# Optimization experiments

Hardware: AMD Instinct MI355X
Metric: run time of the kernel (lower is better)

## Reference

```python
import jax, jax.numpy as jnp
import numpy as np
from jax import lax

B, C, H, W = 4, 256, 64, 64
C8 = C // 8


def _conv1x1(x, w, b):
    # x: (B,C,H,W), w: (O,C) -> (B,O,H,W)
    return jnp.einsum('bchw,oc->bohw', x, w) + b[None, :, None, None]


def setup_inputs() -> dict:
    key = jax.random.key(0)
    ks = jax.random.split(key, 9)
    s1 = 1.0 / np.sqrt(C)          # fan-in scale for 1x1 convs
    sf = 1.0 / np.sqrt(2 * C * 9)  # fan-in scale for 3x3 conv
    return {
        'front_x':     jax.random.normal(ks[0], (B, C, H, W), jnp.float32),
        'cross_x':     jax.random.normal(ks[1], (B, C, H, W), jnp.float32),
        'front_x_hat': jax.random.normal(ks[2], (B, C, H, W), jnp.float32),
        'Wq': jax.random.normal(ks[3], (C8, C), jnp.float32) * s1,
        'bq': jnp.zeros((C8,), jnp.float32),
        'Wk': jax.random.normal(ks[4], (C8, C), jnp.float32) * s1,
        'bk': jnp.zeros((C8,), jnp.float32),
        'Wv': jax.random.normal(ks[5], (C, C), jnp.float32) * s1,
        'bv': jnp.zeros((C,), jnp.float32),
        'Wf': jax.random.normal(ks[6], (C, 2 * C, 3, 3), jnp.float32) * sf,
        'bf': jnp.zeros((C,), jnp.float32),
    }


def reference(front_x, cross_x, front_x_hat, Wq, bq, Wk, bk, Wv, bv, Wf, bf):
    b, c, h, w = front_x.shape
    hw = h * w
    # projections -> (B, C/8, HW)
    q = _conv1x1(cross_x, Wq, bq).reshape(b, -1, hw)
    k = _conv1x1(front_x, Wk, bk).reshape(b, -1, hw)
    # energy[b,i,j] = <key_i, query_j>  (B, HW, HW)
    energy = jnp.einsum('bci,bcj->bij', k, q)
    front_star = jnp.max(energy, axis=1)     # (B, HW) best key score per query
    front_arg = jnp.argmax(energy, axis=1)   # (B, HW) best key index per query
    # value projection and hard gather of best-matching value per position
    v = _conv1x1(front_x_hat, Wv, bv).reshape(b, c, hw)
    T = jnp.take_along_axis(v, front_arg[:, None, :], axis=2).reshape(b, c, h, w)
    S = front_star.reshape(b, 1, h, w)
    cat = jnp.concatenate([front_x, T], axis=1)  # (B, 2C, H, W)
    res = lax.conv_general_dilated(
        cat, Wf, window_strides=(1, 1), padding='SAME',
        dimension_numbers=('NCHW', 'OIHW', 'NCHW')) + bf[None, :, None, None]
    return front_x + res * S
```

## Files before the change

kernel.cpp:

```cpp
#include <hip/hip_runtime.h>

#define Bn 4
#define Cn 256
#define C8 32
#define Hn 64
#define Wn 64
#define HWn 4096
#define PADR 80
#define ROWS (HWn + 2 * PADR)
#define MARGIN 6e-3f

typedef __bf16 bf16x8 __attribute__((ext_vector_type(8)));
typedef float floatx4 __attribute__((ext_vector_type(4)));
typedef unsigned short u16x8 __attribute__((ext_vector_type(8)));

__device__ __forceinline__ unsigned short f2bf(float f) {
  union { float f; unsigned int u; } c; c.f = f;
  unsigned int u = c.u;
  return (unsigned short)((u + 0x7FFFu + ((u >> 16) & 1u)) >> 16);
}
__device__ __forceinline__ float bf2f(unsigned short h) {
  union { unsigned int u; float f; } c; c.u = ((unsigned int)h) << 16;
  return c.f;
}
__device__ __forceinline__ void gl_lds16(const void* g, void* l) {
  __builtin_amdgcn_global_load_lds(
      (__attribute__((address_space(1))) void*)(uintptr_t)g,
      (__attribute__((address_space(3))) void*)(uintptr_t)l, 16, 0, 0);
}

__global__ void prep_w(const float* __restrict__ Wq, const float* __restrict__ Wk,
                       const float* __restrict__ Wv, const float* __restrict__ Wf,
                       float* __restrict__ Wqf, float* __restrict__ Wkf,
                       unsigned short* __restrict__ Wvb, unsigned short* __restrict__ Wfb,
                       int* __restrict__ cnt) {
  size_t t = (size_t)blockIdx.x * 256 + threadIdx.x;
  if (t == 0) cnt[0] = 0;
  if (t < 8192) {
    int o = (int)(t / 256), c = (int)(t % 256);
    Wqf[(size_t)c * 32 + o] = Wq[t];
    Wkf[(size_t)c * 32 + o] = Wk[t];
  }
  if (t < 65536) Wvb[t] = f2bf(Wv[t]);
  if (t < (size_t)9 * 256 * 512) {
    int tap = (int)(t / (256 * 512));
    int rem = (int)(t % (256 * 512));
    int o = rem / 512, ci = rem % 512;
    Wfb[t] = f2bf(Wf[((size_t)o * 512 + ci) * 9 + tap]);
  }
}

__global__ __launch_bounds__(1024) void proj_qk(
    const float* __restrict__ cross_x, const float* __restrict__ front_x,
    const float* __restrict__ Wqf, const float* __restrict__ bq,
    const float* __restrict__ Wkf, const float* __restrict__ bk,
    float* __restrict__ qf, float* __restrict__ kf,
    unsigned short* __restrict__ qhi, unsigned short* __restrict__ qlo,
    unsigned short* __restrict__ khi, unsigned short* __restrict__ klo) {
  int tid = threadIdx.x;
  int lane = tid & 63, wv = tid >> 6;
  int slice = wv & 3;
  int chunk = wv >> 2;
  int j = blockIdx.x * 64 + lane;
  int b = blockIdx.y;
  int z = blockIdx.z;
  const float* x = (z == 0) ? cross_x : front_x;
  const float* Wg = (z == 0) ? Wqf : Wkf;
  const float* bd = (z == 0) ? bq : bk;
  float* outp = (z == 0) ? qf : kf;
  unsigned short* hip_ = (z == 0) ? qhi : khi;
  unsigned short* lop_ = (z == 0) ? qlo : klo;
  int o0 = slice * 8;
  int c0 = chunk * 64;

  __shared__ __align__(16) float Wl[8192];
  __shared__ float part[3 * 4 * 8 * 64];

  for (int u = tid; u < 8192; u += 1024) Wl[u] = Wg[u];
  __syncthreads();

  const float* xb = x + (size_t)b * Cn * HWn + j;
  floatx4 a0 = (floatx4)0.0f, a1 = (floatx4)0.0f;
#pragma unroll 16
  for (int c = c0; c < c0 + 64; ++c) {
    float xv = xb[(size_t)c * HWn];
    floatx4 wa = *reinterpret_cast<const floatx4*>(&Wl[c * 32 + o0]);
    floatx4 wb = *reinterpret_cast<const floatx4*>(&Wl[c * 32 + o0 + 4]);
    a0 += wa * xv;
    a1 += wb * xv;
  }
  if (chunk > 0) {
    float* dst = &part[(((chunk - 1) * 4 + slice) * 8) * 64];
#pragma unroll
    for (int o = 0; o < 4; ++o) { dst[o * 64 + lane] = a0[o]; dst[(o + 4) * 64 + lane] = a1[o]; }
  }
  __syncthreads();
  if (chunk != 0) return;
#pragma unroll
  for (int q = 0; q < 3; ++q) {
    const float* src = &part[((q * 4 + slice) * 8) * 64];
#pragma unroll
    for (int o = 0; o < 4; ++o) { a0[o] += src[o * 64 + lane]; a1[o] += src[(o + 4) * 64 + lane]; }
  }
  float acc[8];
#pragma unroll
  for (int o = 0; o < 4; ++o) { acc[o] = a0[o] + bd[o0 + o]; acc[o + 4] = a1[o] + bd[o0 + 4 + o]; }

  float* op = outp + ((size_t)b * HWn + j) * C8 + o0;
  u16x8 hv, lv;
#pragma unroll
  for (int o = 0; o < 8; ++o) {
    op[o] = acc[o];
    unsigned short h = f2bf(acc[o]);
    hv[o] = h;
    lv[o] = f2bf(acc[o] - bf2f(h));
  }
  *reinterpret_cast<u16x8*>(hip_ + ((size_t)b * HWn + j) * C8 + o0) = hv;
  *reinterpret_cast<u16x8*>(lop_ + ((size_t)b * HWn + j) * C8 + o0) = lv;
}

__global__ __launch_bounds__(1024) void energy_approx(
    const unsigned short* __restrict__ khi, const unsigned short* __restrict__ klo,
    const unsigned short* __restrict__ qhi, const unsigned short* __restrict__ qlo,
    float* __restrict__ star, int* __restrict__ argb,
    int* __restrict__ cnt, int* __restrict__ list) {
  int b = blockIdx.y;
  int j0 = blockIdx.x * 32;
  int tid = threadIdx.x;
  int lane = tid & 63, wv = tid >> 6;
  int lm = lane & 15, lq = lane >> 4;

  __shared__ float bv1S[16][32];
  __shared__ int   bi1S[16][32];
  __shared__ float bv2S[16][32];

  bf16x8 qh[2], ql[2];
#pragma unroll
  for (int s = 0; s < 2; ++s) {
    int j = j0 + s * 16 + lm;
    qh[s] = *reinterpret_cast<const bf16x8*>(qhi + ((size_t)b * HWn + j) * 32 + lq * 8);
    ql[s] = *reinterpret_cast<const bf16x8*>(qlo + ((size_t)b * HWn + j) * 32 + lq * 8);
  }
  const unsigned short* kh_base = khi + (size_t)b * HWn * 32 + lq * 8;
  const unsigned short* kl_base = klo + (size_t)b * HWn * 32 + lq * 8;

  float b1[2], b2[2];
#pragma unroll
  for (int s = 0; s < 2; ++s) { b1[s] = -3.0e38f; b2[s] = -3.0e38f; }

  int ibase = wv * 256;
#pragma unroll 4
  for (int it = 0; it < 16; ++it) {
    int i0 = ibase + it * 16;
    bf16x8 ah = *reinterpret_cast<const bf16x8*>(kh_base + (size_t)(i0 + lm) * 32);
    bf16x8 al = *reinterpret_cast<const bf16x8*>(kl_base + (size_t)(i0 + lm) * 32);
#pragma unroll
    for (int s = 0; s < 2; ++s) {
      floatx4 acc = (floatx4)0.0f;
      acc = __builtin_amdgcn_mfma_f32_16x16x32_bf16(ah, qh[s], acc, 0, 0, 0);
      acc = __builtin_amdgcn_mfma_f32_16x16x32_bf16(ah, ql[s], acc, 0, 0, 0);
      acc = __builtin_amdgcn_mfma_f32_16x16x32_bf16(al, qh[s], acc, 0, 0, 0);
#pragma unroll
      for (int r = 0; r < 4; ++r) {
        unsigned code = (unsigned)(it * 4 + r);
        union { float f; unsigned u; } cv; cv.f = acc[r];
        cv.u = (cv.u & ~63u) | code;
        float vp = cv.f;
        b2[s] = __builtin_amdgcn_fmed3f(vp, b1[s], b2[s]);
        b1[s] = fmaxf(b1[s], vp);
      }
    }
  }
  int i1[2];
#pragma unroll
  for (int s = 0; s < 2; ++s) {
    union { float f; unsigned u; } cv; cv.f = b1[s];
    unsigned code = cv.u & 63u;
    i1[s] = ibase + (int)(code >> 2) * 16 + lq * 4 + (int)(code & 3u);
  }
#pragma unroll
  for (int s = 0; s < 2; ++s) {
#pragma unroll
    for (int m = 16; m <= 32; m <<= 1) {
      float ob1 = __shfl_xor(b1[s], m, 64);
      int oi1 = __shfl_xor(i1[s], m, 64);
      float ob2 = __shfl_xor(b2[s], m, 64);
      float c2;
      if (ob1 > b1[s] || (ob1 == b1[s] && oi1 < i1[s])) {
        c2 = fmaxf(b1[s], ob2);
        b1[s] = ob1; i1[s] = oi1;
      } else {
        c2 = fmaxf(ob1, b2[s]);
      }
      b2[s] = c2;
    }
    if (lq == 0) {
      bv1S[wv][s * 16 + lm] = b1[s];
      bi1S[wv][s * 16 + lm] = i1[s];
      bv2S[wv][s * 16 + lm] = b2[s];
    }
  }
  __syncthreads();
  if (tid < 32) {
    float B1 = bv1S[0][tid];
    int I1 = bi1S[0][tid];
    float B2 = bv2S[0][tid];
#pragma unroll
    for (int w = 1; w < 16; ++w) {
      float v1 = bv1S[w][tid];
      int ii = bi1S[w][tid];
      float v2 = bv2S[w][tid];
      if (v1 > B1) { B2 = fmaxf(B1, v2); B1 = v1; I1 = ii; }
      else B2 = fmaxf(B2, v1);
    }
    size_t o = (size_t)b * HWn + j0 + tid;
    union { float f; unsigned u; } cs; cs.f = B1;
    cs.u &= ~63u;
    star[o] = cs.f;
    argb[o] = I1;
    if (B1 - B2 < MARGIN) {
      int slot = atomicAdd(cnt, 1);
      list[slot] = (b << 12) | (j0 + (int)tid);
    }
  }
}

__global__ __launch_bounds__(256) void recheck(
    const float* __restrict__ qf, const float* __restrict__ kf,
    const int* __restrict__ cnt, const int* __restrict__ list,
    float* __restrict__ star, int* __restrict__ argb) {
  __shared__ double bvS[4];
  __shared__ int biS[4];
  int n = cnt[0];
  int tid = threadIdx.x;
  int lane = tid & 63, wv = tid >> 6;
  for (int idx = blockIdx.x; idx < n; idx += gridDim.x) {
    int e = list[idx];
    int b = e >> 12, j = e & 4095;
    const float* qp = qf + ((size_t)b * HWn + j) * 32;
    double qj[32];
#pragma unroll
    for (int o = 0; o < 32; ++o) qj[o] = (double)qp[o];
    double best = -1.0e300;
    int bi = 1 << 30;
    for (int i = tid; i < HWn; i += 256) {
      const float* kp = kf + ((size_t)b * HWn + i) * 32;
      double s = 0.0;
#pragma unroll
      for (int o = 0; o < 32; ++o) s += (double)kp[o] * qj[o];
      if (s > best) { best = s; bi = i; }
    }
#pragma unroll
    for (int m = 1; m < 64; m <<= 1) {
      double ob = __shfl_xor(best, m, 64);
      int oi = __shfl_xor(bi, m, 64);
      if (ob > best || (ob == best && oi < bi)) { best = ob; bi = oi; }
    }
    if (lane == 0) { bvS[wv] = best; biS[wv] = bi; }
    __syncthreads();
    if (tid == 0) {
#pragma unroll
      for (int w = 1; w < 4; ++w) {
        if (bvS[w] > best || (bvS[w] == best && biS[w] < bi)) {
          best = bvS[w]; bi = biS[w];
        }
      }
      star[(size_t)b * HWn + j] = (float)best;
      argb[(size_t)b * HWn + j] = bi;
    }
    __syncthreads();
  }
}

__global__ __launch_bounds__(256) void cat_fx(
    const float* __restrict__ fx, const float* __restrict__ fxh,
    unsigned short* __restrict__ catC, unsigned short* __restrict__ xht) {
  int j0 = blockIdx.x * 64;
  int ci0 = blockIdx.y * 64;
  int b = blockIdx.z >> 1;
  int which = blockIdx.z & 1;
  int tid = threadIdx.x;
  __shared__ unsigned short tile[64][66];

  const float* src = (which == 0) ? fx : fxh;
  for (int u = tid; u < 4096; u += 256) {
    int cl = u >> 6, hw_l = u & 63;
    tile[cl][hw_l] = f2bf(src[((size_t)(b * Cn + ci0 + cl)) * HWn + j0 + hw_l]);
  }
  __syncthreads();
  if (which == 0) {
    for (int u = tid; u < 4096; u += 256) {
      int hw_l = u >> 6, cl = u & 63;
      catC[((size_t)b * ROWS + PADR + j0 + hw_l) * 512 + ci0 + cl] = tile[cl][hw_l];
    }
  } else {
    for (int u = tid; u < 4096; u += 256) {
      int hw_l = u >> 6, cl = u & 63;
      xht[((size_t)b * HWn + j0 + hw_l) * 256 + ci0 + cl] = tile[cl][hw_l];
    }
  }
}

__global__ __launch_bounds__(256) void proj_v_mfma(
    const unsigned short* __restrict__ xht, const unsigned short* __restrict__ Wvb,
    const float* __restrict__ bv, unsigned short* __restrict__ vbf) {
  int m0 = blockIdx.x * 128;
  int o0 = blockIdx.y * 128;
  int b = blockIdx.z;
  int tid = threadIdx.x;
  int lane = tid & 63, wv = tid >> 6;
  int wm = wv >> 1, wn = wv & 1;
  int lm = lane & 15, lq = lane >> 4;

  union SMu {
    struct { unsigned short A[2][128 * 32]; unsigned short B[2][128 * 32]; } st;
    unsigned short TS[128 * 136];
  };
  __shared__ __align__(16) SMu sm;

  floatx4 acc[4][4];
#pragma unroll
  for (int im = 0; im < 4; ++im)
#pragma unroll
    for (int in = 0; in < 4; ++in) acc[im][in] = (floatx4)0.0f;

  const int srow = lane >> 2;
  const int soff = (((lane & 3) ^ ((lane >> 3) & 3)) * 8);
  const int sa = (lq ^ ((lm >> 1) & 3)) * 8;
  const unsigned short* ag = Wvb + (size_t)o0 * 256;
  const unsigned short* bg = xht + ((size_t)b * HWn + m0) * 256;

  auto STAGE = [&](int buf, int kc) {
#pragma unroll
    for (int i = 0; i < 2; ++i) {
      int r0 = wv * 32 + i * 16;
      gl_lds16(ag + ((size_t)(r0 + srow)) * 256 + kc + soff, &sm.st.A[buf][r0 * 32]);
      gl_lds16(bg + ((size_t)(r0 + srow)) * 256 + kc + soff, &sm.st.B[buf][r0 * 32]);
    }
  };
  auto COMPUTE = [&](int buf) {
    bf16x8 afr[4];
#pragma unroll
    for (int im = 0; im < 4; ++im)
      afr[im] = *reinterpret_cast<const bf16x8*>(
          &sm.st.A[buf][(wm * 64 + im * 16 + lm) * 32 + sa]);
#pragma unroll
    for (int in = 0; in < 4; ++in) {
      bf16x8 bfr = *reinterpret_cast<const bf16x8*>(
          &sm.st.B[buf][(wn * 64 + in * 16 + lm) * 32 + sa]);
#pragma unroll
      for (int im = 0; im < 4; ++im)
        acc[im][in] = __builtin_amdgcn_mfma_f32_16x16x32_bf16(
            afr[im], bfr, acc[im][in], 0, 0, 0);
    }
  };

  STAGE(0, 0);
#pragma unroll 2
  for (int st = 0; st < 8; ++st) {
    __builtin_amdgcn_s_barrier();
    if (st < 7) {
      STAGE((st + 1) & 1, (st + 1) * 32);
      asm volatile("s_waitcnt vmcnt(4)" ::: "memory");
    } else {
      asm volatile("s_waitcnt vmcnt(0)" ::: "memory");
    }
    __builtin_amdgcn_s_barrier();
    __builtin_amdgcn_sched_barrier(0);
    COMPUTE(st & 1);
  }
  __builtin_amdgcn_s_barrier();

#pragma unroll
  for (int in = 0; in < 4; ++in) {
    int pl = wn * 64 + in * 16 + lm;
#pragma unroll
    for (int im = 0; im < 4; ++im) {
#pragma unroll
      for (int r = 0; r < 4; ++r) {
        int ol = wm * 64 + im * 16 + lq * 4 + r;
        sm.TS[pl * 136 + ol] = f2bf(acc[im][in][r] + bv[o0 + ol]);
      }
    }
  }
  __syncthreads();
  for (int idx = tid; idx < 128 * 16; idx += 256) {
    int p = idx >> 4, ch = idx & 15;
    u16x8 val = *reinterpret_cast<const u16x8*>(&sm.TS[p * 136 + ch * 8]);
    *reinterpret_cast<u16x8*>(
        &vbf[((size_t)b * HWn + m0 + p) * 256 + o0 + ch * 8]) = val;
  }
}

__global__ __launch_bounds__(256) void gather_cat(
    const unsigned short* __restrict__ vbf, const int* __restrict__ argb,
    unsigned short* __restrict__ catC) {
  int b = blockIdx.y;
  int tid = threadIdx.x;
  if (blockIdx.x == 16) {
    for (int u = tid; u < 2 * PADR * 512; u += 256) {
      int r = u >> 9;
      int rr = (r < PADR) ? r : (HWn + r);
      catC[((size_t)b * ROWS + rr) * 512 + (u & 511)] = 0;
    }
    return;
  }
  __shared__ int ajS[256];
  int j0 = blockIdx.x * 256;
  ajS[tid] = argb[(size_t)b * HWn + j0 + tid];
  __syncthreads();
#pragma unroll 4
  for (int u = tid; u < 256 * 32; u += 256) {
    int pl = u >> 5, ch = u & 31;
    int aj = ajS[pl];
    u16x8 val = *reinterpret_cast<const u16x8*>(
        &vbf[((size_t)b * HWn + aj) * 256 + ch * 8]);
    *reinterpret_cast<u16x8*>(
        &catC[((size_t)b * ROWS + PADR + j0 + pl) * 512 + 256 + ch * 8]) = val;
  }
}

__global__ __launch_bounds__(256) void conv_mfma(
    const unsigned short* __restrict__ catC, const unsigned short* __restrict__ Wfb,
    const float* __restrict__ fx, const float* __restrict__ bfc,
    const float* __restrict__ star, float* __restrict__ out) {
  int m0 = blockIdx.x * 128;
  int o0 = blockIdx.y * 128;
  int b = blockIdx.z;
  int tid = threadIdx.x;
  int lane = tid & 63;
  int wv = tid >> 6;
  int wm = wv >> 1, wn = wv & 1;
  int lm = lane & 15, lq = lane >> 4;
  const bool lane_first = (lm == 0);
  const bool lane_last = (lm == 15);

  __shared__ __align__(16) unsigned short AS[2][3 * 128 * 32];
  __shared__ __align__(16) unsigned short BS[2][144 * 32];

  floatx4 acc[4][4];
#pragma unroll
  for (int im = 0; im < 4; ++im)
#pragma unroll
    for (int in = 0; in < 4; ++in) acc[im][in] = (floatx4)0.0f;

  const int srow = lane >> 2;
  const int soff = (((lane & 3) ^ ((lane >> 3) & 3)) * 8);
  const int sa = (lq ^ ((lm >> 1) & 3)) * 8;
  const unsigned short* catb = catC + ((size_t)b * ROWS + PADR + m0 - 65) * 512;
  const unsigned short* wfo = Wfb + (size_t)o0 * 512;

  auto STAGE = [&](int buf, int step) {
    int g = step >> 4;
    int kc = (step & 15) * 32;
    if (wv < 3) {
      const unsigned short* at = wfo + (size_t)(g * 3 + wv) * 256 * 512;
#pragma unroll
      for (int s = 0; s < 8; ++s)
        gl_lds16(at + ((size_t)(s * 16 + srow)) * 512 + kc + soff,
                 &AS[buf][(wv * 128 + s * 16) * 32]);
    } else {
      const unsigned short* bt = catb + (size_t)(g * 64) * 512;
#pragma unroll
      for (int s = 0; s < 9; ++s)
        gl_lds16(bt + ((size_t)(s * 16 + srow)) * 512 + kc + soff,
                 &BS[buf][(s * 16) * 32]);
    }
  };
  auto COMPUTE = [&](int buf) {
#pragma unroll
    for (int t = 0; t < 3; ++t) {
      bf16x8 afr[4];
#pragma unroll
      for (int im = 0; im < 4; ++im)
        afr[im] = *reinterpret_cast<const bf16x8*>(
            &AS[buf][(t * 128 + wm * 64 + im * 16 + lm) * 32 + sa]);
#pragma unroll
      for (int in = 0; in < 4; ++in) {
        int u = wn * 64 + in * 16 + lm + t;
        int sb = (lq ^ ((u >> 1) & 3)) * 8;
        u16x8 braw = *reinterpret_cast<const u16x8*>(&BS[buf][u * 32 + sb]);
        if ((t == 0 && in == 0 && lane_first) ||
            (t == 2 && in == 3 && lane_last))
          braw = (u16x8)(unsigned short)0;
        union { u16x8 u8; bf16x8 h; } cvt; cvt.u8 = braw;
#pragma unroll
        for (int im = 0; im < 4; ++im)
          acc[im][in] = __builtin_amdgcn_mfma_f32_16x16x32_bf16(
              afr[im], cvt.h, acc[im][in], 0, 0, 0);
      }
    }
  };

  STAGE(0, 0);
#pragma unroll 2
  for (int st = 0; st < 48; ++st) {
    __builtin_amdgcn_s_barrier();
    if (st < 47) {
      STAGE((st + 1) & 1, st + 1);
      if (wv < 3) asm volatile("s_waitcnt vmcnt(8)" ::: "memory");
      else        asm volatile("s_waitcnt vmcnt(9)" ::: "memory");
    } else {
      asm volatile("s_waitcnt vmcnt(0)" ::: "memory");
    }
    __builtin_amdgcn_s_barrier();
    __builtin_amdgcn_sched_barrier(0);
    COMPUTE(st & 1);
  }

#pragma unroll
  for (int in = 0; in < 4; ++in) {
    int p = m0 + wn * 64 + in * 16 + lm;
    float s = star[(size_t)b * HWn + p];
#pragma unroll
    for (int im = 0; im < 4; ++im) {
      int ob = o0 + wm * 64 + im * 16 + lq * 4;
#pragma unroll
      for (int r = 0; r < 4; ++r) {
        size_t idx = ((size_t)(b * Cn + ob + r)) * HWn + p;
        out[idx] = fx[idx] + (acc[im][in][r] + bfc[ob + r]) * s;
      }
    }
  }
}

extern "C" void kernel_launch(void* const* d_in, const int* in_sizes, int n_in,
                              void* d_out, int out_size, void* d_ws, size_t ws_size,
                              hipStream_t stream) {
  const float* front_x   = (const float*)d_in[0];
  const float* cross_x   = (const float*)d_in[1];
  const float* front_hat = (const float*)d_in[2];
  const float* Wq = (const float*)d_in[3];
  const float* bq = (const float*)d_in[4];
  const float* Wk = (const float*)d_in[5];
  const float* bk = (const float*)d_in[6];
  const float* Wv = (const float*)d_in[7];
  const float* bv = (const float*)d_in[8];
  const float* Wf = (const float*)d_in[9];
  const float* bf = (const float*)d_in[10];
  float* out = (float*)d_out;

  char* ws = (char*)d_ws;
  size_t off = 0;
  auto alloc = [&](size_t bytes) -> void* {
    void* p = (void*)(ws + off);
    off += (bytes + 255) & ~(size_t)255;
    return p;
  };
  float* Wqf = (float*)alloc(8192 * sizeof(float));
  float* Wkf = (float*)alloc(8192 * sizeof(float));
  unsigned short* Wvb = (unsigned short*)alloc(65536 * sizeof(unsigned short));
  unsigned short* Wfb = (unsigned short*)alloc((size_t)9 * 256 * 512 * sizeof(unsigned short));
  float* qf  = (float*)alloc((size_t)Bn * HWn * C8 * sizeof(float));
  float* kf  = (float*)alloc((size_t)Bn * HWn * C8 * sizeof(float));
  unsigned short* qhi = (unsigned short*)alloc((size_t)Bn * HWn * C8 * 2);
  unsigned short* qlo = (unsigned short*)alloc((size_t)Bn * HWn * C8 * 2);
  unsigned short* khi = (unsigned short*)alloc((size_t)Bn * HWn * C8 * 2);
  unsigned short* klo = (unsigned short*)alloc((size_t)Bn * HWn * C8 * 2);
  float*  star = (float*)alloc((size_t)Bn * HWn * sizeof(float));
  int*    argb = (int*)alloc((size_t)Bn * HWn * sizeof(int));
  int*    cnt  = (int*)alloc(256);
  int*    list = (int*)alloc((size_t)Bn * HWn * sizeof(int));
  unsigned short* xht = (unsigned short*)alloc((size_t)Bn * HWn * 256 * 2);
  unsigned short* vbf = (unsigned short*)alloc((size_t)Bn * HWn * 256 * 2);
  unsigned short* catC = (unsigned short*)alloc((size_t)Bn * ROWS * 512 * sizeof(unsigned short));

  prep_w<<<dim3((9 * 256 * 512 + 255) / 256), dim3(256), 0, stream>>>(
      Wq, Wk, Wv, Wf, Wqf, Wkf, Wvb, Wfb, cnt);

  proj_qk<<<dim3(HWn / 64, Bn, 2), dim3(1024), 0, stream>>>(
      cross_x, front_x, Wqf, bq, Wkf, bk, qf, kf, qhi, qlo, khi, klo);

  energy_approx<<<dim3(HWn / 32, Bn), dim3(1024), 0, stream>>>(
      khi, klo, qhi, qlo, star, argb, cnt, list);

  recheck<<<dim3(256), dim3(256), 0, stream>>>(qf, kf, cnt, list, star, argb);

  cat_fx<<<dim3(HWn / 64, Cn / 64, Bn * 2), dim3(256), 0, stream>>>(
      front_x, front_hat, catC, xht);

  proj_v_mfma<<<dim3(HWn / 128, Cn / 128, Bn), dim3(256), 0, stream>>>(
      xht, Wvb, bv, vbf);

  gather_cat<<<dim3(HWn / 256 + 1, Bn), dim3(256), 0, stream>>>(vbf, argb, catC);

  conv_mfma<<<dim3(HWn / 128, Cn / 128, Bn), dim3(256), 0, stream>>>(
      catC, Wfb, front_x, bf, star, out);
}
```

Baseline: 241.8 us.

## Rewrite 3x3 conv MFMA kernel to load operands directly from global, halve pixel tile

Replaces the LDS double-buffered staging pipeline in the conv kernel with direct per-lane global loads of the weight and activation fragments into registers. The pixel tile shrinks from 128 to 64, which doubles the grid and halves the accumulators, and launch bounds request two blocks per SIMD. This removes the LDS traffic and barriers, but it gives up data sharing across waves, so each wave re-reads the same weights and activations from global memory or cache. That raises cache and bandwidth pressure and exposes load latency.

```diff
diff --git a/kernel.cpp b/kernel.cpp
--- a/kernel.cpp
+++ b/kernel.cpp
@@ -420,11 +420,11 @@
   }
 }
 
-__global__ __launch_bounds__(256) void conv_mfma(
+__global__ __launch_bounds__(256, 2) void conv_mfma(
     const unsigned short* __restrict__ catC, const unsigned short* __restrict__ Wfb,
     const float* __restrict__ fx, const float* __restrict__ bfc,
     const float* __restrict__ star, float* __restrict__ out) {
-  int m0 = blockIdx.x * 128;
+  int m0 = blockIdx.x * 64;
   int o0 = blockIdx.y * 128;
   int b = blockIdx.z;
   int tid = threadIdx.x;
@@ -432,85 +432,61 @@
   int wv = tid >> 6;
   int wm = wv >> 1, wn = wv & 1;
   int lm = lane & 15, lq = lane >> 4;
-  const bool lane_first = (lm == 0);
-  const bool lane_last = (lm == 15);
-
-  __shared__ __align__(16) unsigned short AS[2][3 * 128 * 32];
-  __shared__ __align__(16) unsigned short BS[2][144 * 32];
-
-  floatx4 acc[4][4];
+
+  floatx4 acc[4][2];
 #pragma unroll
   for (int im = 0; im < 4; ++im)
 #pragma unroll
-    for (int in = 0; in < 4; ++in) acc[im][in] = (floatx4)0.0f;
-
-  const int srow = lane >> 2;
-  const int soff = (((lane & 3) ^ ((lane >> 3) & 3)) * 8);
-  const int sa = (lq ^ ((lm >> 1) & 3)) * 8;
-  const unsigned short* catb = catC + ((size_t)b * ROWS + PADR + m0 - 65) * 512;
-  const unsigned short* wfo = Wfb + (size_t)o0 * 512;
-
-  auto STAGE = [&](int buf, int step) {
-    int g = step >> 4;
-    int kc = (step & 15) * 32;
-    if (wv < 3) {
-      const unsigned short* at = wfo + (size_t)(g * 3 + wv) * 256 * 512;
-#pragma unroll
-      for (int s = 0; s < 8; ++s)
-        gl_lds16(at + ((size_t)(s * 16 + srow)) * 512 + kc + soff,
-                 &AS[buf][(wv * 128 + s * 16) * 32]);
-    } else {
-      const unsigned short* bt = catb + (size_t)(g * 64) * 512;
-#pragma unroll
-      for (int s = 0; s < 9; ++s)
-        gl_lds16(bt + ((size_t)(s * 16 + srow)) * 512 + kc + soff,
-                 &BS[buf][(s * 16) * 32]);
-    }
-  };
-  auto COMPUTE = [&](int buf) {
-#pragma unroll
-    for (int t = 0; t < 3; ++t) {
-      bf16x8 afr[4];
-#pragma unroll
-      for (int im = 0; im < 4; ++im)
-        afr[im] = *reinterpret_cast<const bf16x8*>(
-            &AS[buf][(t * 128 + wm * 64 + im * 16 + lm) * 32 + sa]);
-#pragma unroll
-      for (int in = 0; in < 4; ++in) {
-        int u = wn * 64 + in * 16 + lm + t;
-        int sb = (lq ^ ((u >> 1) & 3)) * 8;
-        u16x8 braw = *reinterpret_cast<const u16x8*>(&BS[buf][u * 32 + sb]);
-        if ((t == 0 && in == 0 && lane_first) ||
-            (t == 2 && in == 3 && lane_last))
-          braw = (u16x8)(unsigned short)0;
-        union { u16x8 u8; bf16x8 h; } cvt; cvt.u8 = braw;
+    for (int in = 0; in < 2; ++in) acc[im][in] = (floatx4)0.0f;
+
+  const bool e0 = (wn == 0) && (lm == 0);
+  const bool e1 = (wn == 1) && (lm == 15);
+
+  const unsigned short* abase =
+      Wfb + (size_t)(o0 + wm * 64 + lm) * 512 + lq * 8;
+  const unsigned short* bbase =
+      catC + ((size_t)b * ROWS + PADR + m0 + wn * 32 + lm - 65) * 512 + lq * 8;
+
+#pragma unroll
+  for (int g = 0; g < 3; ++g) {
+    const unsigned short* ag = abase + (size_t)(g * 3) * 131072;
+    const unsigned short* bg = bbase + (size_t)(g * 64) * 512;
+#pragma unroll 2
+    for (int kci = 0; kci < 16; ++kci) {
+      const int kc = kci * 32;
+      u16x8 af[3][4], bf_[3][2];
+#pragma unroll
+      for (int t = 0; t < 3; ++t)
 #pragma unroll
         for (int im = 0; im < 4; ++im)
-          acc[im][in] = __builtin_amdgcn_mfma_f32_16x16x32_bf16(
-              afr[im], cvt.h, acc[im][in], 0, 0, 0);
-      }
-    }
-  };
-
-  STAGE(0, 0);
-#pragma unroll 2
-  for (int st = 0; st < 48; ++st) {
-    __builtin_amdgcn_s_barrier();
-    if (st < 47) {
-      STAGE((st + 1) & 1, st + 1);
-      if (wv < 3) asm volatile("s_waitcnt vmcnt(8)" ::: "memory");
-      else        asm volatile("s_waitcnt vmcnt(9)" ::: "memory");
-    } else {
-      asm volatile("s_waitcnt vmcnt(0)" ::: "memory");
-    }
-    __builtin_amdgcn_s_barrier();
-    __builtin_amdgcn_sched_barrier(0);
-    COMPUTE(st & 1);
-  }
-
-#pragma unroll
-  for (int in = 0; in < 4; ++in) {
-    int p = m0 + wn * 64 + in * 16 + lm;
+          af[t][im] = *reinterpret_cast<const u16x8*>(
+              ag + (size_t)t * 131072 + im * 8192 + kc);
+#pragma unroll
+      for (int t = 0; t < 3; ++t)
+#pragma unroll
+        for (int in = 0; in < 2; ++in)
+          bf_[t][in] = *reinterpret_cast<const u16x8*>(
+              bg + (size_t)(t + in * 16) * 512 + kc);
+      if (e0) bf_[0][0] = (u16x8)(unsigned short)0;
+      if (e1) bf_[2][1] = (u16x8)(unsigned short)0;
+#pragma unroll
+      for (int t = 0; t < 3; ++t)
+#pragma unroll
+        for (int in = 0; in < 2; ++in) {
+          union { u16x8 u8; bf16x8 h; } cb; cb.u8 = bf_[t][in];
+#pragma unroll
+          for (int im = 0; im < 4; ++im) {
+            union { u16x8 u8; bf16x8 h; } ca; ca.u8 = af[t][im];
+            acc[im][in] = __builtin_amdgcn_mfma_f32_16x16x32_bf16(
+                ca.h, cb.h, acc[im][in], 0, 0, 0);
+          }
+        }
+    }
+  }
+
+#pragma unroll
+  for (int in = 0; in < 2; ++in) {
+    int p = m0 + wn * 32 + in * 16 + lm;
     float s = star[(size_t)b * HWn + p];
 #pragma unroll
     for (int im = 0; im < 4; ++im) {
@@ -584,6 +560,6 @@
 
   gather_cat<<<dim3(HWn / 256 + 1, Bn), dim3(256), 0, stream>>>(vbf, argb, catC);
 
-  conv_mfma<<<dim3(HWn / 128, Cn / 128, Bn), dim3(256), 0, stream>>>(
+  conv_mfma<<<dim3(HWn / 64, Cn / 128, Bn), dim3(256), 0, stream>>>(
       catC, Wfb, front_x, bf, star, out);
 }
```

After: 389.6 us. 61.1% more time.

## Split 3x3 conv by kernel row with larger tiles and separate combine pass

Applied to the files above, without the earlier changes.

Reworks the conv GEMM to use 256x256 output tiles per 1024-thread block and splits the reduction across the three kernel rows as independent blocks. Each block writes a bf16 partial result, and a new elementwise kernel sums the partials and applies bias, the star scale and the residual. The aim is more operand reuse per LDS tile and better parallelism across the K dimension. The cost is extra global traffic for the partials, an added launch, and lower precision from storing partials in bf16.

```diff
diff --git a/kernel.cpp b/kernel.cpp
--- a/kernel.cpp
+++ b/kernel.cpp
@@ -420,23 +420,21 @@
   }
 }
 
-__global__ __launch_bounds__(256) void conv_mfma(
+__global__ __launch_bounds__(1024) void conv_mfma(
     const unsigned short* __restrict__ catC, const unsigned short* __restrict__ Wfb,
-    const float* __restrict__ fx, const float* __restrict__ bfc,
-    const float* __restrict__ star, float* __restrict__ out) {
-  int m0 = blockIdx.x * 128;
-  int o0 = blockIdx.y * 128;
-  int b = blockIdx.z;
+    unsigned short* __restrict__ Pg) {
+  int m0 = blockIdx.x * 256;
+  int bz = blockIdx.z;
+  int b = bz / 3, g = bz % 3;
+  int dy = g - 1;
   int tid = threadIdx.x;
   int lane = tid & 63;
   int wv = tid >> 6;
-  int wm = wv >> 1, wn = wv & 1;
+  int wm = wv >> 2, wn = wv & 3;
   int lm = lane & 15, lq = lane >> 4;
-  const bool lane_first = (lm == 0);
-  const bool lane_last = (lm == 15);
-
-  __shared__ __align__(16) unsigned short AS[2][3 * 128 * 32];
-  __shared__ __align__(16) unsigned short BS[2][144 * 32];
+
+  __shared__ __align__(16) unsigned short AS[2][3 * 256 * 32];
+  __shared__ __align__(16) unsigned short BS[2][272 * 32];
 
   floatx4 acc[4][4];
 #pragma unroll
@@ -447,24 +445,22 @@
   const int srow = lane >> 2;
   const int soff = (((lane & 3) ^ ((lane >> 3) & 3)) * 8);
   const int sa = (lq ^ ((lm >> 1) & 3)) * 8;
-  const unsigned short* catb = catC + ((size_t)b * ROWS + PADR + m0 - 65) * 512;
-  const unsigned short* wfo = Wfb + (size_t)o0 * 512;
-
-  auto STAGE = [&](int buf, int step) {
-    int g = step >> 4;
-    int kc = (step & 15) * 32;
-    if (wv < 3) {
-      const unsigned short* at = wfo + (size_t)(g * 3 + wv) * 256 * 512;
-#pragma unroll
-      for (int s = 0; s < 8; ++s)
-        gl_lds16(at + ((size_t)(s * 16 + srow)) * 512 + kc + soff,
-                 &AS[buf][(wv * 128 + s * 16) * 32]);
-    } else {
-      const unsigned short* bt = catb + (size_t)(g * 64) * 512;
-#pragma unroll
-      for (int s = 0; s < 9; ++s)
-        gl_lds16(bt + ((size_t)(s * 16 + srow)) * 512 + kc + soff,
+  const unsigned short* catb =
+      catC + ((size_t)b * ROWS + PADR + m0 + dy * 64 - 1) * 512;
+  const unsigned short* wfg = Wfb + (size_t)(g * 3) * 256 * 512;
+
+  auto STAGE = [&](int buf, int kci) {
+    int kc = kci * 32;
+    for (int i = wv; i < 65; i += 16) {
+      if (i < 48) {
+        int t = i >> 4, s = i & 15;
+        gl_lds16(wfg + ((size_t)(t * 256 + s * 16 + srow)) * 512 + kc + soff,
+                 &AS[buf][(t * 256 + s * 16) * 32]);
+      } else {
+        int s = i - 48;
+        gl_lds16(catb + ((size_t)(s * 16 + srow)) * 512 + kc + soff,
                  &BS[buf][(s * 16) * 32]);
+      }
     }
   };
   auto COMPUTE = [&](int buf) {
@@ -474,14 +470,14 @@
 #pragma unroll
       for (int im = 0; im < 4; ++im)
         afr[im] = *reinterpret_cast<const bf16x8*>(
-            &AS[buf][(t * 128 + wm * 64 + im * 16 + lm) * 32 + sa]);
+            &AS[buf][(t * 256 + wm * 64 + im * 16 + lm) * 32 + sa]);
 #pragma unroll
       for (int in = 0; in < 4; ++in) {
         int u = wn * 64 + in * 16 + lm + t;
         int sb = (lq ^ ((u >> 1) & 3)) * 8;
         u16x8 braw = *reinterpret_cast<const u16x8*>(&BS[buf][u * 32 + sb]);
-        if ((t == 0 && in == 0 && lane_first) ||
-            (t == 2 && in == 3 && lane_last))
+        if ((t == 0 && in == 0 && lm == 0) ||
+            (t == 2 && in == 3 && lm == 15))
           braw = (u16x8)(unsigned short)0;
         union { u16x8 u8; bf16x8 h; } cvt; cvt.u8 = braw;
 #pragma unroll
@@ -494,12 +490,12 @@
 
   STAGE(0, 0);
 #pragma unroll 2
-  for (int st = 0; st < 48; ++st) {
+  for (int st = 0; st < 16; ++st) {
+    asm volatile("s_waitcnt lgkmcnt(0)" ::: "memory");
     __builtin_amdgcn_s_barrier();
-    if (st < 47) {
+    if (st < 15) {
       STAGE((st + 1) & 1, st + 1);
-      if (wv < 3) asm volatile("s_waitcnt vmcnt(8)" ::: "memory");
-      else        asm volatile("s_waitcnt vmcnt(9)" ::: "memory");
+      asm volatile("s_waitcnt vmcnt(4)" ::: "memory");
     } else {
       asm volatile("s_waitcnt vmcnt(0)" ::: "memory");
     }
@@ -508,19 +504,48 @@
     COMPUTE(st & 1);
   }
 
+  unsigned short* P = Pg + ((size_t)(g * Bn + b) * Cn) * HWn;
 #pragma unroll
   for (int in = 0; in < 4; ++in) {
     int p = m0 + wn * 64 + in * 16 + lm;
-    float s = star[(size_t)b * HWn + p];
 #pragma unroll
     for (int im = 0; im < 4; ++im) {
-      int ob = o0 + wm * 64 + im * 16 + lq * 4;
-#pragma unroll
-      for (int r = 0; r < 4; ++r) {
-        size_t idx = ((size_t)(b * Cn + ob + r)) * HWn + p;
-        out[idx] = fx[idx] + (acc[im][in][r] + bfc[ob + r]) * s;
-      }
-    }
+      int ob = wm * 64 + im * 16 + lq * 4;
+#pragma unroll
+      for (int r = 0; r < 4; ++r)
+        P[(size_t)(ob + r) * HWn + p] = f2bf(acc[im][in][r]);
+    }
+  }
+}
+
+__global__ __launch_bounds__(256) void combine(
+    const unsigned short* __restrict__ Pg, const float* __restrict__ fx,
+    const float* __restrict__ bf, const float* __restrict__ star,
+    float* __restrict__ out) {
+  size_t e = ((size_t)blockIdx.x * 256 + threadIdx.x) * 8;
+  int p = (int)(e & 4095);
+  int bo = (int)(e >> 12);
+  int o = bo & 255, b = bo >> 8;
+  const size_t gs = (size_t)Bn * Cn * HWn;
+  u16x8 q0 = *reinterpret_cast<const u16x8*>(Pg + e);
+  u16x8 q1 = *reinterpret_cast<const u16x8*>(Pg + gs + e);
+  u16x8 q2 = *reinterpret_cast<const u16x8*>(Pg + 2 * gs + e);
+  float bias = bf[o];
+  const float* sp = star + (size_t)b * HWn + p;
+  const float* fp = fx + e;
+  float* op = out + e;
+#pragma unroll
+  for (int h = 0; h < 2; ++h) {
+    floatx4 s = *reinterpret_cast<const floatx4*>(sp + h * 4);
+    floatx4 f = *reinterpret_cast<const floatx4*>(fp + h * 4);
+    floatx4 r;
+#pragma unroll
+    for (int i = 0; i < 4; ++i) {
+      int k = h * 4 + i;
+      float a = bf2f(q0[k]) + bf2f(q1[k]) + bf2f(q2[k]);
+      r[i] = f[i] + (a + bias) * s[i];
+    }
+    *reinterpret_cast<floatx4*>(op + h * 4) = r;
   }
 }
 
@@ -564,6 +589,7 @@
   unsigned short* xht = (unsigned short*)alloc((size_t)Bn * HWn * 256 * 2);
   unsigned short* vbf = (unsigned short*)alloc((size_t)Bn * HWn * 256 * 2);
   unsigned short* catC = (unsigned short*)alloc((size_t)Bn * ROWS * 512 * sizeof(unsigned short));
+  unsigned short* Pg = (unsigned short*)alloc((size_t)3 * Bn * Cn * HWn * 2);
 
   prep_w<<<dim3((9 * 256 * 512 + 255) / 256), dim3(256), 0, stream>>>(
       Wq, Wk, Wv, Wf, Wqf, Wkf, Wvb, Wfb, cnt);
@@ -584,6 +610,9 @@
 
   gather_cat<<<dim3(HWn / 256 + 1, Bn), dim3(256), 0, stream>>>(vbf, argb, catC);
 
-  conv_mfma<<<dim3(HWn / 128, Cn / 128, Bn), dim3(256), 0, stream>>>(
-      catC, Wfb, front_x, bf, star, out);
-}
+  conv_mfma<<<dim3(HWn / 256, 1, Bn * 3), dim3(1024), 0, stream>>>(
+      catC, Wfb, Pg);
+
+  combine<<<dim3((Bn * Cn * HWn / 8) / 256), dim3(256), 0, stream>>>(
+      Pg, front_x, bf, star, out);
+}
```

Result: slower. 275.2 us (+13.8%).
